# Performance work log

Measured on AMD Instinct MI355X. Metric: run time of the kernel, lower is better.

## Reference

```python
import jax, jax.numpy as jnp
import numpy as np

N_HEADS, D_MODEL, D_HEAD = 16, 1024, 64
EPSILON = -100000.0  # module uses -1e5, not -inf
INIT_STD = 0.02


def setup_inputs() -> dict:
    key = jax.random.key(0)
    ks = jax.random.split(key, 5)
    B, S = 4, 2048
    x = jax.random.normal(ks[0], (B, S, D_MODEL), dtype=jnp.float32)
    W_Q = INIT_STD * jax.random.normal(ks[1], (N_HEADS, D_MODEL, D_HEAD), dtype=jnp.float32)
    W_K = INIT_STD * jax.random.normal(ks[2], (N_HEADS, D_MODEL, D_HEAD), dtype=jnp.float32)
    W_V = INIT_STD * jax.random.normal(ks[3], (N_HEADS, D_MODEL, D_HEAD), dtype=jnp.float32)
    W_O = INIT_STD * jax.random.normal(ks[4], (N_HEADS, D_HEAD, D_MODEL), dtype=jnp.float32)
    b_Q = jnp.zeros((N_HEADS, D_HEAD), jnp.float32)
    b_K = jnp.zeros((N_HEADS, D_HEAD), jnp.float32)
    b_V = jnp.zeros((N_HEADS, D_HEAD), jnp.float32)
    b_O = jnp.zeros((D_MODEL,), jnp.float32)
    return {"normalized_resid_pre": x, "W_Q": W_Q, "b_Q": b_Q, "W_K": W_K,
            "b_K": b_K, "W_V": W_V, "b_V": b_V, "W_O": W_O, "b_O": b_O}


def reference(normalized_resid_pre, W_Q, b_Q, W_K, b_K, W_V, b_V, W_O, b_O):
    x = normalized_resid_pre  # [b, s, e]
    q = jnp.einsum('bse,neh->bsnh', x, W_Q) + b_Q
    k = jnp.einsum('bse,neh->bsnh', x, W_K) + b_K
    v = jnp.einsum('bse,neh->bsnh', x, W_V) + b_V
    scores = jnp.einsum('bqnh,bknh->bnqk', q, k) / jnp.sqrt(jnp.float32(D_HEAD))
    sq, sk = scores.shape[-2], scores.shape[-1]
    causal = jnp.triu(jnp.ones((sq, sk), bool), k=1)  # True above diagonal
    scores = jnp.where(causal, jnp.float32(EPSILON), scores)
    probs = jax.nn.softmax(scores, axis=-1)
    z = jnp.einsum('bnqk,bknh->bqnh', probs, v)
    # sum over heads of per-head output projection + bias
    attn_out = jnp.einsum('bqnh,nhe->bqe', z, W_O) + b_O
    return attn_out
```

## Files before the change

kernel.cpp:

```cpp
#include <hip/hip_runtime.h>


typedef __attribute__((ext_vector_type(8))) short short8;
typedef __attribute__((ext_vector_type(4))) float floatx4;

#define SCL 0.1803368801111244f

__device__ __forceinline__ unsigned short f2bf(float f) {
  unsigned int x = __float_as_uint(f);
  x += 0x7fffu + ((x >> 16) & 1u);
  return (unsigned short)(x >> 16);
}

__device__ __forceinline__ void gload_lds16(const unsigned short* g, unsigned short* lds) {
  __builtin_amdgcn_global_load_lds(
      (const __attribute__((address_space(1))) void*)g,
      (__attribute__((address_space(3))) void*)lds, 16, 0, 0);
}

__global__ __launch_bounds__(256) void prep_kernel(
    const float* __restrict__ X,  unsigned short* __restrict__ Xb,
    const float* __restrict__ Wq, const float* __restrict__ Wk,
    const float* __restrict__ Wv, unsigned short* __restrict__ Bt,
    const float* __restrict__ Wo, unsigned short* __restrict__ Wt)
{
  __shared__ unsigned short T[64 * 72];
  const int bid = blockIdx.x, t = threadIdx.x;
  if (bid < 8192) {
    int idx = ((bid << 8) + t) << 2;
    float4 f = *(const float4*)(X + idx);
    unsigned short u[4] = { f2bf(f.x), f2bf(f.y), f2bf(f.z), f2bf(f.w) };
    *(uint2*)(Xb + idx) = *(uint2*)u;
  } else if (bid < 8960) {
    int b2 = bid - 8192;
    int e0 = (b2 & 15) << 6, nn = (b2 >> 4) & 15, proj = b2 >> 8;
    const float* W = (proj == 0) ? Wq : (proj == 1) ? Wk : Wv;
    const float* src = W + ((size_t)nn << 16) + ((size_t)e0 << 6);
#pragma unroll
    for (int rnd = 0; rnd < 4; ++rnd) {
      int off = (rnd << 10) + (t << 2);
      float4 f = *(const float4*)(src + off);
      int r = off >> 6, h = off & 63;
      T[r * 72 + h]     = f2bf(f.x);
      T[r * 72 + h + 1] = f2bf(f.y);
      T[r * 72 + h + 2] = f2bf(f.z);
      T[r * 72 + h + 3] = f2bf(f.w);
    }
    __syncthreads();
    const int h = t >> 2, ck = t & 3;
    size_t orow = ((size_t)((proj << 10) + (nn << 6) + h) << 10) + e0 + (ck << 4);
#pragma unroll
    for (int g = 0; g < 2; ++g) {
      unsigned short v[8];
#pragma unroll
      for (int j = 0; j < 8; ++j) v[j] = T[((ck << 4) + (g << 3) + j) * 72 + h];
      *(int4*)(Bt + orow + (g << 3)) = *(int4*)v;
    }
  } else {
    int b2 = bid - 8960;
    int e0 = (b2 & 15) << 6, k0 = (b2 >> 4) << 6;
#pragma unroll
    for (int rnd = 0; rnd < 4; ++rnd) {
      int r = (rnd << 4) + (t >> 4);
      int c = (t & 15) << 2;
      float4 f = *(const float4*)(Wo + ((size_t)(k0 + r) << 10) + e0 + c);
      T[r * 72 + c]     = f2bf(f.x);
      T[r * 72 + c + 1] = f2bf(f.y);
      T[r * 72 + c + 2] = f2bf(f.z);
      T[r * 72 + c + 3] = f2bf(f.w);
    }
    __syncthreads();
    const int i = t >> 2, ck = t & 3;
    size_t orow = ((size_t)(e0 + i) << 10) + k0 + (ck << 4);
#pragma unroll
    for (int g = 0; g < 2; ++g) {
      unsigned short v[8];
#pragma unroll
      for (int j = 0; j < 8; ++j) v[j] = T[((ck << 4) + (g << 3) + j) * 72 + i];
      *(int4*)(Wt + orow + (g << 3)) = *(int4*)v;
    }
  }
}

template <int MODE>
__global__ __launch_bounds__(256) void gemm128_kernel(
    const unsigned short* __restrict__ A,
    const unsigned short* __restrict__ Bt,
    const float* __restrict__ b0, const float* __restrict__ b1,
    const float* __restrict__ b2,
    unsigned short* __restrict__ Oq, unsigned short* __restrict__ Ok,
    unsigned short* __restrict__ Ov, float* __restrict__ Of)
{
  const int K = 1024;
  __shared__ __align__(16) unsigned short As[8192];
  __shared__ __align__(16) unsigned short Bs[8192];
  const int tid = threadIdx.x;
  const int l   = tid & 63, w = tid >> 6;
  const int l15 = l & 15,  lg = l >> 4;
  const int mo  = (w >> 1) << 6, no = (w & 1) << 6;
  const int m0  = blockIdx.y << 7, n0 = blockIdx.x << 7;
  const int srow = l >> 3;
  const int gblk = ((l & 7) ^ srow) << 3;
  const int rsw  = l15 & 7;

  floatx4 acc[4][4];
#pragma unroll
  for (int i = 0; i < 4; ++i)
#pragma unroll
    for (int j = 0; j < 4; ++j) acc[i][j] = (floatx4){0.f, 0.f, 0.f, 0.f};

  for (int k0 = 0; k0 < K; k0 += 64) {
    __syncthreads();
#pragma unroll
    for (int s = 0; s < 4; ++s) {
      const int br = (s << 5) + (w << 3);
      gload_lds16(A  + (size_t)(m0 + br + srow) * K + k0 + gblk, &As[br << 6]);
      gload_lds16(Bt + (size_t)(n0 + br + srow) * K + k0 + gblk, &Bs[br << 6]);
    }
    __syncthreads();
#pragma unroll
    for (int kh = 0; kh < 2; ++kh) {
      const int bo = (((kh << 2) + lg) ^ rsw) << 3;
      short8 af[4], bf[4];
#pragma unroll
      for (int mc = 0; mc < 4; ++mc)
        af[mc] = *(const short8*)&As[((mo + (mc << 4) + l15) << 6) + bo];
#pragma unroll
      for (int nc = 0; nc < 4; ++nc)
        bf[nc] = *(const short8*)&Bs[((no + (nc << 4) + l15) << 6) + bo];
#pragma unroll
      for (int mc = 0; mc < 4; ++mc)
#pragma unroll
        for (int nc = 0; nc < 4; ++nc)
          acc[mc][nc] = __builtin_amdgcn_mfma_f32_16x16x32_bf16(af[mc], bf[nc], acc[mc][nc], 0, 0, 0);
    }
  }

#pragma unroll
  for (int nc = 0; nc < 4; ++nc) {
    int c = n0 + no + (nc << 4) + l15;
    if (MODE == 1) {
      float bv = b0[c];
#pragma unroll
      for (int mc = 0; mc < 4; ++mc)
#pragma unroll
        for (int r = 0; r < 4; ++r) {
          int m = m0 + mo + (mc << 4) + (lg << 2) + r;
          Of[((size_t)m << 10) + c] = acc[mc][nc][r] + bv;
        }
    } else {
      int proj = c >> 10, cc = c & 1023;
      int hn = cc >> 6, h = cc & 63;
      const float* bp = (proj == 0) ? b0 : (proj == 1) ? b1 : b2;
      float bv = bp[cc];
      float sc = (proj == 0) ? SCL : 1.0f;
      if (proj < 2) {
        unsigned short* O = (proj == 0) ? Oq : Ok;
#pragma unroll
        for (int mc = 0; mc < 4; ++mc)
#pragma unroll
          for (int r = 0; r < 4; ++r) {
            int m = m0 + mo + (mc << 4) + (lg << 2) + r;
            int bb = m >> 11, ss = m & 2047;
            O[((((size_t)(bb << 4) + hn) << 11) + ss) * 64 + h] = f2bf((acc[mc][nc][r] + bv) * sc);
          }
      } else {
#pragma unroll
        for (int mc = 0; mc < 4; ++mc) {
          int m = m0 + mo + (mc << 4) + (lg << 2);
          int bb = m >> 11, ss = m & 2047;
          unsigned short p0 = f2bf(acc[mc][nc][0] + bv);
          unsigned short p1 = f2bf(acc[mc][nc][1] + bv);
          unsigned short p2 = f2bf(acc[mc][nc][2] + bv);
          unsigned short p3 = f2bf(acc[mc][nc][3] + bv);
          uint2 pk;
          pk.x = (unsigned int)p0 | ((unsigned int)p1 << 16);
          pk.y = (unsigned int)p2 | ((unsigned int)p3 << 16);
          *(uint2*)&Ov[((((size_t)(bb << 4) + hn) << 6) + h) * 2048 + ss] = pk;
        }
      }
    }
  }
}

__global__ __launch_bounds__(256, 3) void flash10_kernel(
    const unsigned short* __restrict__ Q,
    const unsigned short* __restrict__ K,
    const unsigned short* __restrict__ Vt,
    unsigned short* __restrict__ Z)
{
  __shared__ __align__(16) unsigned short Ks[8192];
  __shared__ __align__(16) unsigned short Vs[8192];
  __shared__ __align__(16) unsigned short Ps[8192];

  const int tid = threadIdx.x;
  const int l   = tid & 63, w = tid >> 6;
  const int l15 = l & 15,  lg = l >> 4;
  const int x    = blockIdx.x;
  const int pidx = x >> 6;
  const int head = x & 63;
  const int n = head & 15, b = head >> 4;
  const size_t hoff = (size_t)head << 17;
  const unsigned short* Qh = Q + hoff;
  const unsigned short* Kh = K + hoff;
  const unsigned short* Vh = Vt + hoff;
  unsigned short* Psw = Ps + (w << 11);

  const int srow8 = l >> 3;
  const int sblk8 = ((l & 7) ^ srow8) << 3;
  const int swz   = l15 & 7;
  const int bo0   = (lg ^ swz) << 3;
  const int bo1   = ((4 + lg) ^ swz) << 3;

  const unsigned short* gK = Kh + (size_t)(((w << 4) + srow8) << 6) + sblk8;
  const unsigned short* gV = Vh + (size_t)(((w << 4) + srow8) << 11) + sblk8;
  unsigned short* ldsK0 = &Ks[w << 10];
  unsigned short* ldsV0 = &Vs[w << 10];

  uint2* pw[2][4];
  const short8* pr[2][2];
#pragma unroll
  for (int qc = 0; qc < 2; ++qc) {
    const int rbase = ((qc << 4) + l15) << 6;
#pragma unroll
    for (int mc = 0; mc < 4; ++mc)
      pw[qc][mc] = (uint2*)&Psw[rbase + (((((mc << 1) + (lg >> 1)) ^ swz) << 3) + ((lg & 1) << 2))];
#pragma unroll
    for (int kc = 0; kc < 2; ++kc)
      pr[qc][kc] = (const short8*)&Psw[rbase + ((((kc << 2) + lg) ^ swz) << 3)];
  }

  short8 onef;
#pragma unroll
  for (int i = 0; i < 8; ++i) onef[i] = (short)0x3F80;

  floatx4 z4 = (floatx4){0.f, 0.f, 0.f, 0.f};
  asm volatile("" : "+v"(z4));

  gload_lds16(gK,         ldsK0);
  gload_lds16(gK + 512,   ldsK0 + 512);
  gload_lds16(gV,         ldsV0);
  gload_lds16(gV + 16384, ldsV0 + 512);
  asm volatile("s_waitcnt vmcnt(0)" ::: "memory");
  __builtin_amdgcn_s_barrier();

  int buf = 0;
  for (int half = 0; half < 2; ++half) {
    const int qt  = half ? pidx : (15 - pidx);
    const int q0w = (qt << 7) + (w << 5);

    short8 qf[2][2];
#pragma unroll
    for (int qc = 0; qc < 2; ++qc)
#pragma unroll
      for (int dh = 0; dh < 2; ++dh)
        qf[qc][dh] = *(const short8*)(Qh + (size_t)(q0w + (qc << 4) + l15) * 64 + (dh << 5) + (lg << 3));

    floatx4 acc_o[2][4], acc_l[2];
#pragma unroll
    for (int qc = 0; qc < 2; ++qc) {
      acc_l[qc] = (floatx4){0.f, 0.f, 0.f, 0.f};
#pragma unroll
      for (int dc = 0; dc < 4; ++dc) acc_o[qc][dc] = (floatx4){0.f, 0.f, 0.f, 0.f};
    }

    const int nkt = (qt << 1) + 2;
    for (int kt = 0; kt < nkt; ++kt) {
      const int k0 = kt << 6;

      const int nk0 = (kt + 1 < nkt) ? ((kt + 1) << 6) : (half == 0 ? 0 : -1);
      if (nk0 >= 0) {
        const int nb = (buf ^ 1) << 12;
        const unsigned short* pK = gK + ((size_t)nk0 << 6);
        gload_lds16(pK,       ldsK0 + nb);
        gload_lds16(pK + 512, ldsK0 + nb + 512);
        const unsigned short* pV = gV + nk0;
        gload_lds16(pV,         ldsV0 + nb);
        gload_lds16(pV + 16384, ldsV0 + nb + 512);
      }

      const bool active = (k0 <= q0w + 31);
      if (active) {
        const int cb = buf << 12;

        floatx4 s0[4], s1[4];
        __builtin_amdgcn_s_setprio(1);
#pragma unroll
        for (int mc = 0; mc < 4; ++mc) {
          short8 ak = *(const short8*)&Ks[cb + (((mc << 4) + l15) << 6) + bo0];
          s0[mc] = __builtin_amdgcn_mfma_f32_16x16x32_bf16(ak, qf[0][0], z4, 0, 0, 0);
          s1[mc] = __builtin_amdgcn_mfma_f32_16x16x32_bf16(ak, qf[1][0], z4, 0, 0, 0);
        }
#pragma unroll
        for (int mc = 0; mc < 4; ++mc) {
          short8 ak = *(const short8*)&Ks[cb + (((mc << 4) + l15) << 6) + bo1];
          s0[mc] = __builtin_amdgcn_mfma_f32_16x16x32_bf16(ak, qf[0][1], s0[mc], 0, 0, 0);
          s1[mc] = __builtin_amdgcn_mfma_f32_16x16x32_bf16(ak, qf[1][1], s1[mc], 0, 0, 0);
        }
        __builtin_amdgcn_s_setprio(0);

        const bool needmask = (k0 + 63 > q0w);
#pragma unroll
        for (int qc = 0; qc < 2; ++qc) {
          const int qg = q0w + (qc << 4) + l15;
#pragma unroll
          for (int mc = 0; mc < 4; ++mc) {
            float p[4];
#pragma unroll
            for (int r = 0; r < 4; ++r) {
              float e = exp2f(qc ? s1[mc][r] : s0[mc][r]);
              if (needmask) {
                int key = k0 + (mc << 4) + (lg << 2) + r;
                e = (key > qg) ? 0.f : e;
              }
              p[r] = e;
            }
            uint2 pk;
            asm("v_cvt_pk_bf16_f32 %0, %1, %2" : "=v"(pk.x) : "v"(p[0]), "v"(p[1]));
            asm("v_cvt_pk_bf16_f32 %0, %1, %2" : "=v"(pk.y) : "v"(p[2]), "v"(p[3]));
            *pw[qc][mc] = pk;
          }
        }

        short8 pa[2][2];
#pragma unroll
        for (int qc = 0; qc < 2; ++qc)
#pragma unroll
          for (int kc = 0; kc < 2; ++kc)
            pa[qc][kc] = *pr[qc][kc];
        __builtin_amdgcn_s_setprio(1);
#pragma unroll
        for (int kc = 0; kc < 2; ++kc) {
          const int bo = kc ? bo1 : bo0;
#pragma unroll
          for (int dc = 0; dc < 4; ++dc) {
            short8 vb = *(const short8*)&Vs[cb + (((dc << 4) + l15) << 6) + bo];
            acc_o[0][dc] = __builtin_amdgcn_mfma_f32_16x16x32_bf16(pa[0][kc], vb, acc_o[0][dc], 0, 0, 0);
            acc_o[1][dc] = __builtin_amdgcn_mfma_f32_16x16x32_bf16(pa[1][kc], vb, acc_o[1][dc], 0, 0, 0);
          }
          acc_l[0] = __builtin_amdgcn_mfma_f32_16x16x32_bf16(pa[0][kc], onef, acc_l[0], 0, 0, 0);
          acc_l[1] = __builtin_amdgcn_mfma_f32_16x16x32_bf16(pa[1][kc], onef, acc_l[1], 0, 0, 0);
        }
        __builtin_amdgcn_s_setprio(0);
      }

      asm volatile("s_waitcnt vmcnt(0)" ::: "memory");
      __builtin_amdgcn_s_barrier();
      buf ^= 1;
    }

#pragma unroll
    for (int qc = 0; qc < 2; ++qc) {
      floatx4 inv;
#pragma unroll
      for (int r = 0; r < 4; ++r) inv[r] = 1.f / acc_l[qc][r];
#pragma unroll
      for (int dc = 0; dc < 4; ++dc)
#pragma unroll
        for (int r = 0; r < 4; ++r) {
          int qg = q0w + (qc << 4) + (lg << 2) + r;
          Z[(((size_t)b << 11) + qg) * 1024 + (n << 6) + (dc << 4) + l15] =
              f2bf(acc_o[qc][dc][r] * inv[r]);
        }
    }
  }
}

extern "C" void kernel_launch(void* const* d_in, const int* in_sizes, int n_in,
                              void* d_out, int out_size, void* d_ws, size_t ws_size,
                              hipStream_t stream) {
  const float* x   = (const float*)d_in[0];
  const float* W_Q = (const float*)d_in[1];
  const float* b_Q = (const float*)d_in[2];
  const float* W_K = (const float*)d_in[3];
  const float* b_K = (const float*)d_in[4];
  const float* W_V = (const float*)d_in[5];
  const float* b_V = (const float*)d_in[6];
  const float* W_O = (const float*)d_in[7];
  const float* b_O = (const float*)d_in[8];
  float* out = (float*)d_out;

  unsigned short* ws    = (unsigned short*)d_ws;
  unsigned short* BtQKV = ws;
  unsigned short* Wo_t  = BtQKV + (3u << 20);
  unsigned short* Xb    = Wo_t + (1u << 20);
  unsigned short* Qb    = Xb + (8u << 20);
  unsigned short* Kb    = Qb + (8u << 20);
  unsigned short* Vtb   = Kb + (8u << 20);
  unsigned short* Zb    = Vtb + (8u << 20);

  prep_kernel<<<9216, 256, 0, stream>>>(x, Xb, W_Q, W_K, W_V, BtQKV, W_O, Wo_t);

  gemm128_kernel<0><<<dim3(24, 64), 256, 0, stream>>>(
      Xb, BtQKV, b_Q, b_K, b_V, Qb, Kb, Vtb, nullptr);

  flash10_kernel<<<512, 256, 0, stream>>>(Qb, Kb, Vtb, Zb);

  gemm128_kernel<1><<<dim3(8, 64), 256, 0, stream>>>(
      Zb, Wo_t, b_O, nullptr, nullptr, nullptr, nullptr, nullptr, out);
}
```

Before: 271.1 us.

## Rewrite flash attention with 32x32 MFMA, register-resident P, and one q-tile per block

The attention kernel switches from 16x16x32 to 32x32x16 bf16 MFMAs. The S accumulator layout is reused directly as the A operand for the PV product by repacking with v_permlane32_swap, which removes the LDS round-trip for P and its shared buffer. Each block now handles a single query tile instead of a paired heavy/light tile, so the grid doubles to 1024 blocks, and launch bounds are raised to 4 blocks per CU. This trades the explicit causal load-balancing pairing for more blocks and lower LDS use, and adds cross-lane swap instructions.

```diff
diff --git a/kernel.cpp b/kernel.cpp
--- a/kernel.cpp
+++ b/kernel.cpp
@@ -3,6 +3,7 @@
 
 typedef __attribute__((ext_vector_type(8))) short short8;
 typedef __attribute__((ext_vector_type(4))) float floatx4;
+typedef __attribute__((ext_vector_type(16))) float floatx16;
 
 #define SCL 0.1803368801111244f
 
@@ -183,7 +184,7 @@
   }
 }
 
-__global__ __launch_bounds__(256, 3) void flash10_kernel(
+__global__ __launch_bounds__(256, 4) void flash11_kernel(
     const unsigned short* __restrict__ Q,
     const unsigned short* __restrict__ K,
     const unsigned short* __restrict__ Vt,
@@ -191,51 +192,53 @@
 {
   __shared__ __align__(16) unsigned short Ks[8192];
   __shared__ __align__(16) unsigned short Vs[8192];
-  __shared__ __align__(16) unsigned short Ps[8192];
 
   const int tid = threadIdx.x;
   const int l   = tid & 63, w = tid >> 6;
-  const int l15 = l & 15,  lg = l >> 4;
+  const int l31 = l & 31,  hi = l >> 5;
   const int x    = blockIdx.x;
-  const int pidx = x >> 6;
+  const int qt   = 15 - (x >> 6);
   const int head = x & 63;
   const int n = head & 15, b = head >> 4;
   const size_t hoff = (size_t)head << 17;
   const unsigned short* Qh = Q + hoff;
   const unsigned short* Kh = K + hoff;
   const unsigned short* Vh = Vt + hoff;
-  unsigned short* Psw = Ps + (w << 11);
 
   const int srow8 = l >> 3;
   const int sblk8 = ((l & 7) ^ srow8) << 3;
-  const int swz   = l15 & 7;
-  const int bo0   = (lg ^ swz) << 3;
-  const int bo1   = ((4 + lg) ^ swz) << 3;
+  const int r7    = l31 & 7;
+  const int rowoff = l31 << 6;
+
+  int koff[4];
+#pragma unroll
+  for (int c = 0; c < 4; ++c) koff[c] = ((((c << 1) + hi) ^ r7) << 3);
 
   const unsigned short* gK = Kh + (size_t)(((w << 4) + srow8) << 6) + sblk8;
   const unsigned short* gV = Vh + (size_t)(((w << 4) + srow8) << 11) + sblk8;
   unsigned short* ldsK0 = &Ks[w << 10];
   unsigned short* ldsV0 = &Vs[w << 10];
 
-  uint2* pw[2][4];
-  const short8* pr[2][2];
-#pragma unroll
-  for (int qc = 0; qc < 2; ++qc) {
-    const int rbase = ((qc << 4) + l15) << 6;
-#pragma unroll
-    for (int mc = 0; mc < 4; ++mc)
-      pw[qc][mc] = (uint2*)&Psw[rbase + (((((mc << 1) + (lg >> 1)) ^ swz) << 3) + ((lg & 1) << 2))];
-#pragma unroll
-    for (int kc = 0; kc < 2; ++kc)
-      pr[qc][kc] = (const short8*)&Psw[rbase + ((((kc << 2) + lg) ^ swz) << 3)];
-  }
-
   short8 onef;
 #pragma unroll
   for (int i = 0; i < 8; ++i) onef[i] = (short)0x3F80;
 
-  floatx4 z4 = (floatx4){0.f, 0.f, 0.f, 0.f};
-  asm volatile("" : "+v"(z4));
+  floatx16 z16;
+#pragma unroll
+  for (int i = 0; i < 16; ++i) z16[i] = 0.f;
+  asm volatile("" : "+v"(z16));
+
+  const int q0w = (qt << 7) + (w << 5);
+  const int qg  = q0w + l31;
+
+  short8 qf[4];
+#pragma unroll
+  for (int c = 0; c < 4; ++c)
+    qf[c] = *(const short8*)(Qh + (size_t)qg * 64 + (c << 4) + (hi << 3));
+
+  floatx16 acc_o[2], acc_l;
+#pragma unroll
+  for (int i = 0; i < 16; ++i) { acc_o[0][i] = 0.f; acc_o[1][i] = 0.f; acc_l[i] = 0.f; }
 
   gload_lds16(gK,         ldsK0);
   gload_lds16(gK + 512,   ldsK0 + 512);
@@ -245,125 +248,95 @@
   __builtin_amdgcn_s_barrier();
 
   int buf = 0;
-  for (int half = 0; half < 2; ++half) {
-    const int qt  = half ? pidx : (15 - pidx);
-    const int q0w = (qt << 7) + (w << 5);
-
-    short8 qf[2][2];
-#pragma unroll
-    for (int qc = 0; qc < 2; ++qc)
-#pragma unroll
-      for (int dh = 0; dh < 2; ++dh)
-        qf[qc][dh] = *(const short8*)(Qh + (size_t)(q0w + (qc << 4) + l15) * 64 + (dh << 5) + (lg << 3));
-
-    floatx4 acc_o[2][4], acc_l[2];
-#pragma unroll
-    for (int qc = 0; qc < 2; ++qc) {
-      acc_l[qc] = (floatx4){0.f, 0.f, 0.f, 0.f};
-#pragma unroll
-      for (int dc = 0; dc < 4; ++dc) acc_o[qc][dc] = (floatx4){0.f, 0.f, 0.f, 0.f};
-    }
-
-    const int nkt = (qt << 1) + 2;
-    for (int kt = 0; kt < nkt; ++kt) {
-      const int k0 = kt << 6;
-
-      const int nk0 = (kt + 1 < nkt) ? ((kt + 1) << 6) : (half == 0 ? 0 : -1);
-      if (nk0 >= 0) {
-        const int nb = (buf ^ 1) << 12;
-        const unsigned short* pK = gK + ((size_t)nk0 << 6);
-        gload_lds16(pK,       ldsK0 + nb);
-        gload_lds16(pK + 512, ldsK0 + nb + 512);
-        const unsigned short* pV = gV + nk0;
-        gload_lds16(pV,         ldsV0 + nb);
-        gload_lds16(pV + 16384, ldsV0 + nb + 512);
+  const int nkt = (qt << 1) + 2;
+  for (int kt = 0; kt < nkt; ++kt) {
+    const int k0 = kt << 6;
+
+    if (kt + 1 < nkt) {
+      const int nk0 = (kt + 1) << 6;
+      const int nb = (buf ^ 1) << 12;
+      const unsigned short* pK = gK + ((size_t)nk0 << 6);
+      gload_lds16(pK,       ldsK0 + nb);
+      gload_lds16(pK + 512, ldsK0 + nb + 512);
+      const unsigned short* pV = gV + nk0;
+      gload_lds16(pV,         ldsV0 + nb);
+      gload_lds16(pV + 16384, ldsV0 + nb + 512);
+    }
+
+    if (k0 <= q0w + 31) {
+      const int cb = buf << 12;
+      const bool needmask = (k0 + 63 > q0w);
+
+#pragma unroll
+      for (int kc2 = 0; kc2 < 2; ++kc2) {
+        const int kbase = cb + (kc2 << 11) + rowoff;
+
+        floatx16 s;
+        __builtin_amdgcn_s_setprio(1);
+        {
+          short8 ak = *(const short8*)&Ks[kbase + koff[0]];
+          s = __builtin_amdgcn_mfma_f32_32x32x16_bf16(ak, qf[0], z16, 0, 0, 0);
+        }
+#pragma unroll
+        for (int c = 1; c < 4; ++c) {
+          short8 ak = *(const short8*)&Ks[kbase + koff[c]];
+          s = __builtin_amdgcn_mfma_f32_32x32x16_bf16(ak, qf[c], s, 0, 0, 0);
+        }
+        __builtin_amdgcn_s_setprio(0);
+
+        float p[16];
+#pragma unroll
+        for (int r = 0; r < 16; ++r) {
+          float e = exp2f(s[r]);
+          if (needmask) {
+            int key = k0 + (kc2 << 5) + (r & 3) + ((r >> 2) << 3) + (hi << 2);
+            e = (key > qg) ? 0.f : e;
+          }
+          p[r] = e;
+        }
+
+#pragma unroll
+        for (int cc = 0; cc < 2; ++cc) {
+          const int o = cc << 3;
+          unsigned int w0, w1, w2, w3;
+          asm("v_cvt_pk_bf16_f32 %0, %1, %2" : "=v"(w0) : "v"(p[o + 0]), "v"(p[o + 1]));
+          asm("v_cvt_pk_bf16_f32 %0, %1, %2" : "=v"(w2) : "v"(p[o + 4]), "v"(p[o + 5]));
+          asm volatile("v_permlane32_swap_b32 %0, %1" : "+v"(w0), "+v"(w2));
+          asm("v_cvt_pk_bf16_f32 %0, %1, %2" : "=v"(w1) : "v"(p[o + 2]), "v"(p[o + 3]));
+          asm("v_cvt_pk_bf16_f32 %0, %1, %2" : "=v"(w3) : "v"(p[o + 6]), "v"(p[o + 7]));
+          asm volatile("v_permlane32_swap_b32 %0, %1" : "+v"(w1), "+v"(w3));
+          union { unsigned int u[4]; short8 v; } pu;
+          pu.u[0] = w0; pu.u[1] = w1; pu.u[2] = w2; pu.u[3] = w3;
+          const short8 pa = pu.v;
+
+          const int c = (kc2 << 1) + cc;
+          __builtin_amdgcn_s_setprio(1);
+          short8 vb0 = *(const short8*)&Vs[cb + rowoff + koff[c]];
+          acc_o[0] = __builtin_amdgcn_mfma_f32_32x32x16_bf16(pa, vb0, acc_o[0], 0, 0, 0);
+          short8 vb1 = *(const short8*)&Vs[cb + rowoff + 2048 + koff[c]];
+          acc_o[1] = __builtin_amdgcn_mfma_f32_32x32x16_bf16(pa, vb1, acc_o[1], 0, 0, 0);
+          acc_l = __builtin_amdgcn_mfma_f32_32x32x16_bf16(pa, onef, acc_l, 0, 0, 0);
+          __builtin_amdgcn_s_setprio(0);
+        }
       }
-
-      const bool active = (k0 <= q0w + 31);
-      if (active) {
-        const int cb = buf << 12;
-
-        floatx4 s0[4], s1[4];
-        __builtin_amdgcn_s_setprio(1);
-#pragma unroll
-        for (int mc = 0; mc < 4; ++mc) {
-          short8 ak = *(const short8*)&Ks[cb + (((mc << 4) + l15) << 6) + bo0];
-          s0[mc] = __builtin_amdgcn_mfma_f32_16x16x32_bf16(ak, qf[0][0], z4, 0, 0, 0);
-          s1[mc] = __builtin_amdgcn_mfma_f32_16x16x32_bf16(ak, qf[1][0], z4, 0, 0, 0);
-        }
-#pragma unroll
-        for (int mc = 0; mc < 4; ++mc) {
-          short8 ak = *(const short8*)&Ks[cb + (((mc << 4) + l15) << 6) + bo1];
-          s0[mc] = __builtin_amdgcn_mfma_f32_16x16x32_bf16(ak, qf[0][1], s0[mc], 0, 0, 0);
-          s1[mc] = __builtin_amdgcn_mfma_f32_16x16x32_bf16(ak, qf[1][1], s1[mc], 0, 0, 0);
-        }
-        __builtin_amdgcn_s_setprio(0);
-
-        const bool needmask = (k0 + 63 > q0w);
-#pragma unroll
-        for (int qc = 0; qc < 2; ++qc) {
-          const int qg = q0w + (qc << 4) + l15;
-#pragma unroll
-          for (int mc = 0; mc < 4; ++mc) {
-            float p[4];
-#pragma unroll
-            for (int r = 0; r < 4; ++r) {
-              float e = exp2f(qc ? s1[mc][r] : s0[mc][r]);
-              if (needmask) {
-                int key = k0 + (mc << 4) + (lg << 2) + r;
-                e = (key > qg) ? 0.f : e;
-              }
-              p[r] = e;
-            }
-            uint2 pk;
-            asm("v_cvt_pk_bf16_f32 %0, %1, %2" : "=v"(pk.x) : "v"(p[0]), "v"(p[1]));
-            asm("v_cvt_pk_bf16_f32 %0, %1, %2" : "=v"(pk.y) : "v"(p[2]), "v"(p[3]));
-            *pw[qc][mc] = pk;
-          }
-        }
-
-        short8 pa[2][2];
-#pragma unroll
-        for (int qc = 0; qc < 2; ++qc)
-#pragma unroll
-          for (int kc = 0; kc < 2; ++kc)
-            pa[qc][kc] = *pr[qc][kc];
-        __builtin_amdgcn_s_setprio(1);
-#pragma unroll
-        for (int kc = 0; kc < 2; ++kc) {
-          const int bo = kc ? bo1 : bo0;
-#pragma unroll
-          for (int dc = 0; dc < 4; ++dc) {
-            short8 vb = *(const short8*)&Vs[cb + (((dc << 4) + l15) << 6) + bo];
-            acc_o[0][dc] = __builtin_amdgcn_mfma_f32_16x16x32_bf16(pa[0][kc], vb, acc_o[0][dc], 0, 0, 0);
-            acc_o[1][dc] = __builtin_amdgcn_mfma_f32_16x16x32_bf16(pa[1][kc], vb, acc_o[1][dc], 0, 0, 0);
-          }
-          acc_l[0] = __builtin_amdgcn_mfma_f32_16x16x32_bf16(pa[0][kc], onef, acc_l[0], 0, 0, 0);
-          acc_l[1] = __builtin_amdgcn_mfma_f32_16x16x32_bf16(pa[1][kc], onef, acc_l[1], 0, 0, 0);
-        }
-        __builtin_amdgcn_s_setprio(0);
-      }
-
-      asm volatile("s_waitcnt vmcnt(0)" ::: "memory");
-      __builtin_amdgcn_s_barrier();
-      buf ^= 1;
-    }
-
-#pragma unroll
-    for (int qc = 0; qc < 2; ++qc) {
-      floatx4 inv;
-#pragma unroll
-      for (int r = 0; r < 4; ++r) inv[r] = 1.f / acc_l[qc][r];
-#pragma unroll
-      for (int dc = 0; dc < 4; ++dc)
-#pragma unroll
-        for (int r = 0; r < 4; ++r) {
-          int qg = q0w + (qc << 4) + (lg << 2) + r;
-          Z[(((size_t)b << 11) + qg) * 1024 + (n << 6) + (dc << 4) + l15] =
-              f2bf(acc_o[qc][dc][r] * inv[r]);
-        }
-    }
+    }
+
+    asm volatile("s_waitcnt vmcnt(0)" ::: "memory");
+    __builtin_amdgcn_s_barrier();
+    buf ^= 1;
   }
+
+  float inv[16];
+#pragma unroll
+  for (int r = 0; r < 16; ++r) inv[r] = 1.f / acc_l[r];
+#pragma unroll
+  for (int dc = 0; dc < 2; ++dc)
+#pragma unroll
+    for (int r = 0; r < 16; ++r) {
+      int qrow = q0w + (r & 3) + ((r >> 2) << 3) + (hi << 2);
+      Z[(((size_t)b << 11) + qrow) * 1024 + (n << 6) + (dc << 5) + l31] =
+          f2bf(acc_o[dc][r] * inv[r]);
+    }
 }
 
 extern "C" void kernel_launch(void* const* d_in, const int* in_sizes, int n_in,
@@ -394,7 +367,7 @@
   gemm128_kernel<0><<<dim3(24, 64), 256, 0, stream>>>(
       Xb, BtQKV, b_Q, b_K, b_V, Qb, Kb, Vtb, nullptr);
 
-  flash10_kernel<<<512, 256, 0, stream>>>(Qb, Kb, Vtb, Zb);
+  flash11_kernel<<<1024, 256, 0, stream>>>(Qb, Kb, Vtb, Zb);
 
   gemm128_kernel<1><<<dim3(8, 64), 256, 0, stream>>>(
       Zb, Wo_t, b_O, nullptr, nullptr, nullptr, nullptr, nullptr, out);
```

After: 267.8 us. Within noise of the previous version (-1.2%).
